# Optimization experiments

Measured on AMD Instinct MI355X. Metric: run time of the kernel, lower is better.

Reference implementation:

```python
import jax, jax.numpy as jnp
import numpy as np

B, S, D = 2, 2048, 1024
H = 16
DH = D // H
FFN = 4096
EPS = 1e-5
SCALE = 1.0 / np.sqrt(DH).astype(np.float32)


def layer_norm(x, g, b):
    mu = jnp.mean(x, axis=-1, keepdims=True)
    var = jnp.mean(jnp.square(x - mu), axis=-1, keepdims=True)
    return (x - mu) * jax.lax.rsqrt(var + EPS) * g + b


def setup_inputs() -> dict:
    key = jax.random.key(0)
    ks = jax.random.split(key, 12)
    std = 0.02
    return {
        "x": jax.random.normal(ks[0], (B, S, D), dtype=jnp.float32),
        "mask": jax.random.randint(ks[1], (B, S), 0, 2, dtype=jnp.int32),
        "w_qkv": jax.random.normal(ks[2], (D, 3 * D), dtype=jnp.float32) * std,
        "w_out": jax.random.normal(ks[3], (D, D), dtype=jnp.float32) * std,
        "b_out": jnp.zeros((D,), dtype=jnp.float32),
        "g1": jnp.ones((D,), dtype=jnp.float32),
        "be1": jnp.zeros((D,), dtype=jnp.float32),
        "g2": jnp.ones((D,), dtype=jnp.float32),
        "be2": jnp.zeros((D,), dtype=jnp.float32),
        "w1": jax.random.normal(ks[4], (D, FFN), dtype=jnp.float32) * std,
        "b1": jnp.zeros((FFN,), dtype=jnp.float32),
        "w2": jax.random.normal(ks[5], (FFN, D), dtype=jnp.float32) * std,
        "b2": jnp.zeros((D,), dtype=jnp.float32),
    }


def reference(x, mask, w_qkv, w_out, b_out, g1, be1, g2, be2, w1, b1, w2, b2):
    # --- pre-norm self-attention ---
    h = layer_norm(x, g1, be1)                              # [B,S,D]
    qkv = (h @ w_qkv).reshape(B, S, 3, H, DH)               # [B,S,3,H,Dh]
    q, k, v = [jnp.transpose(qkv[:, :, i], (0, 2, 1, 3)) for i in range(3)]  # [B,H,S,Dh]
    scores = jnp.einsum("bhqd,bhkd->bhqk", q, k) * SCALE    # [B,H,S,S]
    key_mask = (mask != 0)[:, None, None, :]                # [B,1,1,S]
    scores = jnp.where(key_mask, scores, -1e9)
    attn = jax.nn.softmax(scores, axis=-1)
    out = jnp.einsum("bhqk,bhkd->bhqd", attn, v)            # [B,H,S,Dh]
    out = jnp.transpose(out, (0, 2, 1, 3)).reshape(B, S, D)
    x = x + (out @ w_out + b_out)
    # --- pre-norm FFN ---
    h2 = layer_norm(x, g2, be2)
    ffn = jax.nn.relu(h2 @ w1 + b1) @ w2 + b2
    return x + ffn
```

## Files before the change

kernel.cpp:

```cpp
#include <hip/hip_runtime.h>

typedef unsigned short u16;
typedef __bf16 bf16x8 __attribute__((ext_vector_type(8)));
typedef float f32x4 __attribute__((ext_vector_type(4)));

typedef __attribute__((address_space(1))) const void* as1cv;
typedef __attribute__((address_space(3))) void* as3v;

__device__ __forceinline__ u16 f2bf(float f) {
  union { float f; unsigned u; } v;
  v.f = f;
  unsigned r = (v.u + 0x7fffu + ((v.u >> 16) & 1u)) >> 16;
  return (u16)r;
}

__device__ __forceinline__ unsigned cvtpk(float lo, float hi) {
  unsigned r;
  asm("v_cvt_pk_bf16_f32 %0, %1, %2" : "=v"(r) : "v"(lo), "v"(hi));
  return r;
}

__device__ __forceinline__ void gload16(const void* g, void* l) {
  __builtin_amdgcn_global_load_lds((as1cv)g, (as3v)l, 16, 0, 0);
}

__global__ __launch_bounds__(256)
void ln_kernel(const float* __restrict__ x, const float* __restrict__ g,
               const float* __restrict__ be, u16* __restrict__ out) {
  __shared__ float red[8];
  const int row = blockIdx.x;
  const int tid = threadIdx.x;
  const float4 v = ((const float4*)(x + (size_t)row * 1024))[tid];
  float s = v.x + v.y + v.z + v.w;
#pragma unroll
  for (int off = 1; off < 64; off <<= 1) s += __shfl_xor(s, off, 64);
  const int wv = tid >> 6, lane = tid & 63;
  if (lane == 0) red[wv] = s;
  __syncthreads();
  s = red[0] + red[1] + red[2] + red[3];
  const float mu = s * (1.0f / 1024.0f);
  const float d0 = v.x - mu, d1 = v.y - mu, d2 = v.z - mu, d3 = v.w - mu;
  float q = d0 * d0 + d1 * d1 + d2 * d2 + d3 * d3;
#pragma unroll
  for (int off = 1; off < 64; off <<= 1) q += __shfl_xor(q, off, 64);
  if (lane == 0) red[4 + wv] = q;
  __syncthreads();
  q = red[4] + red[5] + red[6] + red[7];
  const float inv = rsqrtf(q * (1.0f / 1024.0f) + 1e-5f);
  const float4 gv = ((const float4*)g)[tid];
  const float4 bv = ((const float4*)be)[tid];
  unsigned p0 = (unsigned)f2bf(d0 * inv * gv.x + bv.x) |
                ((unsigned)f2bf(d1 * inv * gv.y + bv.y) << 16);
  unsigned p1 = (unsigned)f2bf(d2 * inv * gv.z + bv.z) |
                ((unsigned)f2bf(d3 * inv * gv.w + bv.w) << 16);
  uint2 o; o.x = p0; o.y = p1;
  *(uint2*)(out + (size_t)row * 1024 + tid * 4) = o;
}

__global__ __launch_bounds__(256)
void transpose_all(const float* __restrict__ i0, u16* __restrict__ o0,
                   const float* __restrict__ i1, u16* __restrict__ o1,
                   const float* __restrict__ i2, u16* __restrict__ o2,
                   const float* __restrict__ i3, u16* __restrict__ o3) {
  __shared__ float t[32][33];
  int id = blockIdx.x;
  const float* in; u16* out; int K, N, nx;
  if (id < 3072)      { in = i0; out = o0; K = 1024; N = 3072; nx = 96; }
  else if (id < 4096) { id -= 3072; in = i1; out = o1; K = 1024; N = 1024; nx = 32; }
  else if (id < 8192) { id -= 4096; in = i2; out = o2; K = 1024; N = 4096; nx = 128; }
  else                { id -= 8192; in = i3; out = o3; K = 4096; N = 1024; nx = 32; }
  const int n0 = (id % nx) * 32, k0 = (id / nx) * 32;
  const int tx = threadIdx.x & 31, ty = threadIdx.x >> 5;
  for (int r = ty; r < 32; r += 8)
    t[r][tx] = in[(size_t)(k0 + r) * N + n0 + tx];
  __syncthreads();
  for (int r = ty; r < 32; r += 8)
    out[(size_t)(n0 + r) * K + k0 + tx] = f2bf(t[tx][r]);
}

__global__ __launch_bounds__(256, 3)
void gemm64(const u16* __restrict__ A, const u16* __restrict__ Bt,
            const float* __restrict__ bias, const float* __restrict__ res,
            float* __restrict__ C, int M, int N, int K) {
  __shared__ u16 As[4][4096];
  __shared__ u16 Bs[4][2048];
  const int tid = threadIdx.x;
  const int wv = tid >> 6, lane = tid & 63;
  const int bm = blockIdx.x * 128;
  const int bn = blockIdx.y * 64;
  const int wr = wv >> 1, wc = wv & 1;
  const int l16 = lane & 15, lh = lane >> 4;

  const int ssk = ((lane & 3) ^ ((lane >> 3) & 3)) << 3;
  const int rdk = (lh ^ ((l16 >> 1) & 3)) << 3;

  f32x4 acc[4][2] = {};

  const u16* Ag = A + (size_t)(bm + wv * 16 + (lane >> 2)) * K + ssk;
  const u16* Bg = Bt + (size_t)(bn + wv * 16 + (lane >> 2)) * K + ssk;

#define STG_A64(buf, ko)  do { \
    gload16(Ag + (ko), &As[buf][wv * 512]); \
    gload16(Ag + (size_t)64 * K + (ko), &As[buf][2048 + wv * 512]); } while (0)
#define STG_B64(buf, ko)  do { \
    gload16(Bg + (ko), &Bs[buf][wv * 512]); } while (0)

  const int nst = K >> 5;
  STG_A64(0, 0); STG_B64(0, 0);
  STG_A64(1, 32); STG_B64(1, 32);
  STG_A64(2, 64); STG_B64(2, 64);

  for (int t = 0; t < nst; ++t) {
    const int cur = t & 3;
    const int rem = nst - t;
    if (rem >= 3)      asm volatile("s_waitcnt vmcnt(6)" ::: "memory");
    else if (rem == 2) asm volatile("s_waitcnt vmcnt(3)" ::: "memory");
    else               asm volatile("s_waitcnt vmcnt(0)" ::: "memory");
    __builtin_amdgcn_s_barrier();
    asm volatile("" ::: "memory");
    const int nxb = (t + 3) & 3;
    bf16x8 af[4], bfv[2];
#pragma unroll
    for (int i = 0; i < 4; i++)
      af[i] = *(const bf16x8*)&As[cur][(wr * 64 + i * 16 + l16) * 32 + rdk];
    bfv[0] = *(const bf16x8*)&Bs[cur][(wc * 32 + l16) * 32 + rdk];
    if (t + 3 < nst) STG_A64(nxb, (t + 3) * 32);
    __builtin_amdgcn_s_setprio(1);
#pragma unroll
    for (int i = 0; i < 4; i++)
      acc[i][0] = __builtin_amdgcn_mfma_f32_16x16x32_bf16(af[i], bfv[0], acc[i][0], 0, 0, 0);
    __builtin_amdgcn_s_setprio(0);
    bfv[1] = *(const bf16x8*)&Bs[cur][(wc * 32 + 16 + l16) * 32 + rdk];
    if (t + 3 < nst) STG_B64(nxb, (t + 3) * 32);
    __builtin_amdgcn_s_setprio(1);
#pragma unroll
    for (int i = 0; i < 4; i++)
      acc[i][1] = __builtin_amdgcn_mfma_f32_16x16x32_bf16(af[i], bfv[1], acc[i][1], 0, 0, 0);
    __builtin_amdgcn_s_setprio(0);
  }
#undef STG_A64
#undef STG_B64

#pragma unroll
  for (int i = 0; i < 4; i++) {
#pragma unroll
    for (int j = 0; j < 2; j++) {
      const int col = bn + wc * 32 + j * 16 + l16;
      const float bv = bias[col];
#pragma unroll
      for (int r = 0; r < 4; r++) {
        const int row = bm + wr * 64 + i * 16 + lh * 4 + r;
        const float v = acc[i][j][r] + bv + res[(size_t)row * N + col];
        C[(size_t)row * N + col] = v;
      }
    }
  }
}

template<int BIAS, int RELU, int MODE>
__global__ __launch_bounds__(512, 2)
void gemm256(const u16* __restrict__ A, const u16* __restrict__ Bt,
             const float* __restrict__ bias, u16* __restrict__ C,
             u16* __restrict__ vt, int M, int N, int K) {
  __shared__ u16 As[2][16384];
  __shared__ u16 Bs[2][16384];
  const int tid = threadIdx.x;
  const int wv = tid >> 6, lane = tid & 63;
  const int l16 = lane & 15, lh = lane >> 4;
  const int wm = wv >> 2, wn = wv & 3;
  const int bm = blockIdx.x * 256, bn = blockIdx.y * 256;

  const int koff = ((lane & 7) ^ ((lane >> 3) & 7)) << 3;
  const int ka0 = ((lh ^ (l16 & 7)) << 3);
  const int ka1 = (((4 + lh) ^ (l16 & 7)) << 3);

  f32x4 acc[8][4] = {};

  const u16* Ag = A + (size_t)(bm + wv * 8 + (lane >> 3)) * K + koff;
  const u16* Bg = Bt + (size_t)(bn + wv * 8 + (lane >> 3)) * K + koff;

#define STAGE256(buf, ko)                                                  \
  do {                                                                     \
    _Pragma("unroll")                                                      \
    for (int j = 0; j < 4; ++j) {                                          \
      gload16(Ag + (size_t)(j * 64) * K + (ko), &As[buf][j * 4096 + wv * 512]); \
      gload16(Bg + (size_t)(j * 64) * K + (ko), &Bs[buf][j * 4096 + wv * 512]); \
    }                                                                      \
  } while (0)

  const int nt = K >> 6;
  STAGE256(0, 0);
  if (nt > 1) STAGE256(1, 64);

  for (int t = 0; t < nt; ++t) {
    const int cur = t & 1;
    if (t + 1 < nt) asm volatile("s_waitcnt vmcnt(8)" ::: "memory");
    else            asm volatile("s_waitcnt vmcnt(0)" ::: "memory");
    __builtin_amdgcn_s_barrier();
    asm volatile("" ::: "memory");
#pragma unroll
    for (int kk = 0; kk < 2; ++kk) {
      const int ko = kk ? ka1 : ka0;
      bf16x8 af[8], bfv[4];
#pragma unroll
      for (int i = 0; i < 8; ++i)
        af[i] = *(const bf16x8*)&As[cur][(wm * 128 + i * 16 + l16) * 64 + ko];
#pragma unroll
      for (int n = 0; n < 4; ++n)
        bfv[n] = *(const bf16x8*)&Bs[cur][(wn * 64 + n * 16 + l16) * 64 + ko];
      __builtin_amdgcn_s_setprio(1);
#pragma unroll
      for (int i = 0; i < 8; ++i)
#pragma unroll
        for (int n = 0; n < 4; ++n)
          acc[i][n] = __builtin_amdgcn_mfma_f32_16x16x32_bf16(af[i], bfv[n], acc[i][n], 0, 0, 0);
      __builtin_amdgcn_s_setprio(0);
    }
    asm volatile("" ::: "memory");
    __builtin_amdgcn_s_barrier();
    asm volatile("" ::: "memory");
    if (t + 2 < nt) STAGE256(cur, (t + 2) * 64);
  }
#undef STAGE256

#pragma unroll
  for (int i = 0; i < 8; ++i)
#pragma unroll
    for (int n = 0; n < 4; ++n) {
      const int col = bn + wn * 64 + n * 16 + l16;
      const float bv = BIAS ? bias[col] : 0.0f;
      if (MODE == 3 && bn >= 2048) {
        const int cc = col - 2048, h = cc >> 6, d = cc & 63;
        const int row0 = bm + wm * 128 + i * 16 + lh * 4;
        const int bb = row0 >> 11, kv0 = row0 & 2047;
        const int p0 = (kv0 & 32) | (((kv0 >> 2) & 3) << 3) | (((kv0 >> 4) & 1) << 2);
        uint2 o;
        o.x = (unsigned)f2bf(acc[i][n][0]) | ((unsigned)f2bf(acc[i][n][1]) << 16);
        o.y = (unsigned)f2bf(acc[i][n][2]) | ((unsigned)f2bf(acc[i][n][3]) << 16);
        *(uint2*)(vt + ((size_t)(bb * 16 + h) * 64 + d) * 2048 + (kv0 & ~63) + p0) = o;
      } else {
#pragma unroll
        for (int r = 0; r < 4; ++r) {
          const int row = bm + wm * 128 + i * 16 + lh * 4 + r;
          float v = acc[i][n][r] + bv;
          if (RELU) v = fmaxf(v, 0.0f);
          C[(size_t)row * N + col] = f2bf(v);
        }
      }
    }
}

__global__ __launch_bounds__(256, 4)
void attn3(const u16* __restrict__ qkv, const u16* __restrict__ vT,
           const int* __restrict__ mask, u16* __restrict__ aout) {
  __shared__ u16 KsS[2][4096];
  __shared__ u16 VsS[2][4096];
  __shared__ float mbL[2048];

  const int tid = threadIdx.x;
  const int wv = tid >> 6, lane = tid & 63;
  const int l16 = lane & 15, lh = lane >> 4;
  const int bh = blockIdx.x, b = bh >> 4, h = bh & 15;
  const int q0 = blockIdx.y * 64 + wv * 16;

  {
    const int4* srcm = (const int4*)(mask + b * 2048);
    float4* dstm = (float4*)mbL;
#pragma unroll
    for (int u = 0; u < 2; ++u) {
      const int4 mv = srcm[tid + u * 256];
      float4 f;
      f.x = mv.x ? 0.f : -1.4426950408889634e9f;
      f.y = mv.y ? 0.f : -1.4426950408889634e9f;
      f.z = mv.z ? 0.f : -1.4426950408889634e9f;
      f.w = mv.w ? 0.f : -1.4426950408889634e9f;
      dstm[tid + u * 256] = f;
    }
  }

  bf16x8 qf[2];
#pragma unroll
  for (int c = 0; c < 2; ++c)
    qf[c] = *(const bf16x8*)(qkv + (size_t)(b * 2048 + q0 + l16) * 3072 + h * 64 + c * 32 + 8 * lh);

  const int rs = (l16 & 7) << 4;
  const int koff0 = ((16 * lh) ^ rs) >> 1;
  const int koff1 = ((64 + 16 * lh) ^ rs) >> 1;
  const int voff0 = koff0, voff1 = koff1;

  const int rl0 = wv * 8 + (lane >> 3);
  const int rl1 = 32 + wv * 8 + (lane >> 3);
  const int glog = (lane & 7) ^ ((lane >> 3) & 7);
  const u16* kg0 = qkv + (size_t)(b * 2048 + rl0) * 3072 + 1024 + h * 64 + 8 * glog;
  const u16* kg1 = qkv + (size_t)(b * 2048 + rl1) * 3072 + 1024 + h * 64 + 8 * glog;
  const u16* vg0 = vT + ((size_t)bh * 64 + rl0) * 2048 + 8 * glog;
  const u16* vg1 = vT + ((size_t)bh * 64 + rl1) * 2048 + 8 * glog;

  gload16(kg0, &KsS[0][wv * 512]);
  gload16(kg1, &KsS[0][2048 + wv * 512]);
  gload16(vg0, &VsS[0][wv * 512]);
  gload16(vg1, &VsS[0][2048 + wv * 512]);
  kg0 += 64 * 3072; kg1 += 64 * 3072; vg0 += 64; vg1 += 64;

  const float CL2 = 0.125f * 1.4426950408889634f;
  f32x4 lsum = {};
  f32x4 oT[4] = {};
  union U8 { unsigned u[4]; bf16x8 v; };
  U8 onesu;
  onesu.u[0] = onesu.u[1] = onesu.u[2] = onesu.u[3] = 0x3F803F80u;
  const bf16x8 ones = onesu.v;

  for (int t = 0; t < 32; ++t) {
    asm volatile("s_waitcnt vmcnt(0)" ::: "memory");
    __syncthreads();
    const int cur = t & 1;
    if (t + 1 < 32) {
      const int nx = cur ^ 1;
      gload16(kg0, &KsS[nx][wv * 512]);
      gload16(kg1, &KsS[nx][2048 + wv * 512]);
      gload16(vg0, &VsS[nx][wv * 512]);
      gload16(vg1, &VsS[nx][2048 + wv * 512]);
      kg0 += 64 * 3072; kg1 += 64 * 3072; vg0 += 64; vg1 += 64;
    }

    const u16* Kb = &KsS[cur][0];
    const u16* Vb = &VsS[cur][0];

    f32x4 mbc[4];
#pragma unroll
    for (int n = 0; n < 4; ++n)
      mbc[n] = *(const f32x4*)&mbL[t * 64 + n * 16 + 4 * lh];

    f32x4 s[4] = {};
    __builtin_amdgcn_s_setprio(1);
#pragma unroll
    for (int c = 0; c < 2; ++c) {
      const int ko = c ? koff1 : koff0;
      bf16x8 kf[4];
#pragma unroll
      for (int n = 0; n < 4; ++n)
        kf[n] = *(const bf16x8*)(Kb + (n * 16 + l16) * 64 + ko);
#pragma unroll
      for (int n = 0; n < 4; ++n)
        s[n] = __builtin_amdgcn_mfma_f32_16x16x32_bf16(kf[n], qf[c], s[n], 0, 0, 0);
    }
    __builtin_amdgcn_s_setprio(0);

#pragma unroll
    for (int n = 0; n < 4; ++n)
#pragma unroll
      for (int j = 0; j < 4; ++j)
        s[n][j] = __builtin_exp2f(fmaf(s[n][j], CL2, mbc[n][j]));

    U8 pa[2];
#pragma unroll
    for (int u = 0; u < 2; ++u) {
      pa[u].u[0] = cvtpk(s[2 * u][0], s[2 * u][1]);
      pa[u].u[1] = cvtpk(s[2 * u][2], s[2 * u][3]);
      pa[u].u[2] = cvtpk(s[2 * u + 1][0], s[2 * u + 1][1]);
      pa[u].u[3] = cvtpk(s[2 * u + 1][2], s[2 * u + 1][3]);
    }

    __builtin_amdgcn_s_setprio(1);
#pragma unroll
    for (int u = 0; u < 2; ++u) {
      const int vo = u ? voff1 : voff0;
      lsum = __builtin_amdgcn_mfma_f32_16x16x32_bf16(ones, pa[u].v, lsum, 0, 0, 0);
#pragma unroll
      for (int D = 0; D < 4; ++D) {
        const bf16x8 va = *(const bf16x8*)(Vb + (D * 16 + l16) * 64 + vo);
        oT[D] = __builtin_amdgcn_mfma_f32_16x16x32_bf16(va, pa[u].v, oT[D], 0, 0, 0);
      }
    }
    __builtin_amdgcn_s_setprio(0);
  }

  const float rr = 1.0f / lsum[0];
#pragma unroll
  for (int D = 0; D < 4; ++D) {
    uint2 o;
    o.x = cvtpk(oT[D][0] * rr, oT[D][1] * rr);
    o.y = cvtpk(oT[D][2] * rr, oT[D][3] * rr);
    *(uint2*)(aout + (size_t)(b * 2048 + q0 + l16) * 1024 + h * 64 + D * 16 + 4 * lh) = o;
  }
}

extern "C" void kernel_launch(void* const* d_in, const int* in_sizes, int n_in,
                              void* d_out, int out_size, void* d_ws, size_t ws_size,
                              hipStream_t stream) {
  (void)in_sizes; (void)n_in; (void)out_size; (void)ws_size;
  const float* x     = (const float*)d_in[0];
  const int*   mask  = (const int*)d_in[1];
  const float* w_qkv = (const float*)d_in[2];
  const float* w_out = (const float*)d_in[3];
  const float* b_out = (const float*)d_in[4];
  const float* g1    = (const float*)d_in[5];
  const float* be1   = (const float*)d_in[6];
  const float* g2    = (const float*)d_in[7];
  const float* be2   = (const float*)d_in[8];
  const float* w1    = (const float*)d_in[9];
  const float* b1    = (const float*)d_in[10];
  const float* w2    = (const float*)d_in[11];
  const float* b2    = (const float*)d_in[12];
  float* out = (float*)d_out;

  char* ws = (char*)d_ws;
  u16* hA    = (u16*)(ws);
  u16* wqkvT = (u16*)(ws + 8388608);
  u16* woutT = (u16*)(ws + 14680064);
  u16* w1T   = (u16*)(ws + 16777216);
  u16* w2T   = (u16*)(ws + 25165824);
  u16* qkv   = (u16*)(ws + 33554432);
  u16* ffn1  = (u16*)(ws + 33554432);
  u16* vTb   = (u16*)(ws + 67108864);
  u16* aout  = (u16*)(ws + 75497472);

  ln_kernel<<<4096, 256, 0, stream>>>(x, g1, be1, hA);
  transpose_all<<<12288, 256, 0, stream>>>(w_qkv, wqkvT, w_out, woutT, w1, w1T, w2, w2T);
  gemm256<0, 0, 3><<<dim3(16, 12), 512, 0, stream>>>(hA, wqkvT, nullptr, qkv, vTb, 4096, 3072, 1024);
  attn3<<<dim3(32, 32), 256, 0, stream>>>(qkv, vTb, mask, aout);
  gemm64<<<dim3(32, 16), 256, 0, stream>>>(aout, woutT, b_out, x, out, 4096, 1024, 1024);
  ln_kernel<<<4096, 256, 0, stream>>>(out, g2, be2, hA);
  gemm256<1, 1, 1><<<dim3(16, 16), 512, 0, stream>>>(hA, w1T, b1, ffn1, nullptr, 4096, 4096, 1024);
  gemm64<<<dim3(32, 16), 256, 0, stream>>>(ffn1, w2T, b2, out, out, 4096, 1024, 4096);
}
```

Before: 240.5 us.

## Process two query sub-tiles per wave in attention to reuse K/V fragments

Each wave now handles 32 query rows (two 16-row sub-tiles) instead of 16, so every block covers 128 queries and the grid along queries is halved. K and V fragments read from LDS and the staged global tiles are reused across both sub-tiles, cutting LDS reads and global K/V traffic per query. In exchange register use doubles for accumulators and scores, so launch bounds drop to two blocks per SM, and there are only half as many blocks (512) to fill the device.

```diff
diff --git a/kernel.cpp b/kernel.cpp
--- a/kernel.cpp
+++ b/kernel.cpp
@@ -250,8 +250,8 @@
     }
 }
 
-__global__ __launch_bounds__(256, 4)
-void attn3(const u16* __restrict__ qkv, const u16* __restrict__ vT,
+__global__ __launch_bounds__(256, 2)
+void attn4(const u16* __restrict__ qkv, const u16* __restrict__ vT,
            const int* __restrict__ mask, u16* __restrict__ aout) {
   __shared__ u16 KsS[2][4096];
   __shared__ u16 VsS[2][4096];
@@ -261,7 +261,7 @@
   const int wv = tid >> 6, lane = tid & 63;
   const int l16 = lane & 15, lh = lane >> 4;
   const int bh = blockIdx.x, b = bh >> 4, h = bh & 15;
-  const int q0 = blockIdx.y * 64 + wv * 16;
+  const int q0 = blockIdx.y * 128 + wv * 32;
 
   {
     const int4* srcm = (const int4*)(mask + b * 2048);
@@ -278,10 +278,12 @@
     }
   }
 
-  bf16x8 qf[2];
-#pragma unroll
-  for (int c = 0; c < 2; ++c)
-    qf[c] = *(const bf16x8*)(qkv + (size_t)(b * 2048 + q0 + l16) * 3072 + h * 64 + c * 32 + 8 * lh);
+  bf16x8 qf[2][2];
+#pragma unroll
+  for (int qb = 0; qb < 2; ++qb)
+#pragma unroll
+    for (int c = 0; c < 2; ++c)
+      qf[qb][c] = *(const bf16x8*)(qkv + (size_t)(b * 2048 + q0 + qb * 16 + l16) * 3072 + h * 64 + c * 32 + 8 * lh);
 
   const int rs = (l16 & 7) << 4;
   const int koff0 = ((16 * lh) ^ rs) >> 1;
@@ -303,8 +305,8 @@
   kg0 += 64 * 3072; kg1 += 64 * 3072; vg0 += 64; vg1 += 64;
 
   const float CL2 = 0.125f * 1.4426950408889634f;
-  f32x4 lsum = {};
-  f32x4 oT[4] = {};
+  f32x4 lsum[2] = {};
+  f32x4 oT[4][2] = {};
   union U8 { unsigned u[4]; bf16x8 v; };
   U8 onesu;
   onesu.u[0] = onesu.u[1] = onesu.u[2] = onesu.u[3] = 0x3F803F80u;
@@ -331,7 +333,7 @@
     for (int n = 0; n < 4; ++n)
       mbc[n] = *(const f32x4*)&mbL[t * 64 + n * 16 + 4 * lh];
 
-    f32x4 s[4] = {};
+    f32x4 s[2][4] = {};
     __builtin_amdgcn_s_setprio(1);
 #pragma unroll
     for (int c = 0; c < 2; ++c) {
@@ -341,47 +343,58 @@
       for (int n = 0; n < 4; ++n)
         kf[n] = *(const bf16x8*)(Kb + (n * 16 + l16) * 64 + ko);
 #pragma unroll
+      for (int qb = 0; qb < 2; ++qb)
+#pragma unroll
+        for (int n = 0; n < 4; ++n)
+          s[qb][n] = __builtin_amdgcn_mfma_f32_16x16x32_bf16(kf[n], qf[qb][c], s[qb][n], 0, 0, 0);
+    }
+    __builtin_amdgcn_s_setprio(0);
+
+#pragma unroll
+    for (int qb = 0; qb < 2; ++qb)
+#pragma unroll
       for (int n = 0; n < 4; ++n)
-        s[n] = __builtin_amdgcn_mfma_f32_16x16x32_bf16(kf[n], qf[c], s[n], 0, 0, 0);
-    }
-    __builtin_amdgcn_s_setprio(0);
-
-#pragma unroll
-    for (int n = 0; n < 4; ++n)
-#pragma unroll
-      for (int j = 0; j < 4; ++j)
-        s[n][j] = __builtin_exp2f(fmaf(s[n][j], CL2, mbc[n][j]));
-
-    U8 pa[2];
-#pragma unroll
-    for (int u = 0; u < 2; ++u) {
-      pa[u].u[0] = cvtpk(s[2 * u][0], s[2 * u][1]);
-      pa[u].u[1] = cvtpk(s[2 * u][2], s[2 * u][3]);
-      pa[u].u[2] = cvtpk(s[2 * u + 1][0], s[2 * u + 1][1]);
-      pa[u].u[3] = cvtpk(s[2 * u + 1][2], s[2 * u + 1][3]);
-    }
+#pragma unroll
+        for (int j = 0; j < 4; ++j)
+          s[qb][n][j] = __builtin_exp2f(fmaf(s[qb][n][j], CL2, mbc[n][j]));
+
+    U8 pa[2][2];
+#pragma unroll
+    for (int qb = 0; qb < 2; ++qb)
+#pragma unroll
+      for (int u = 0; u < 2; ++u) {
+        pa[qb][u].u[0] = cvtpk(s[qb][2 * u][0], s[qb][2 * u][1]);
+        pa[qb][u].u[1] = cvtpk(s[qb][2 * u][2], s[qb][2 * u][3]);
+        pa[qb][u].u[2] = cvtpk(s[qb][2 * u + 1][0], s[qb][2 * u + 1][1]);
+        pa[qb][u].u[3] = cvtpk(s[qb][2 * u + 1][2], s[qb][2 * u + 1][3]);
+      }
 
     __builtin_amdgcn_s_setprio(1);
 #pragma unroll
     for (int u = 0; u < 2; ++u) {
       const int vo = u ? voff1 : voff0;
-      lsum = __builtin_amdgcn_mfma_f32_16x16x32_bf16(ones, pa[u].v, lsum, 0, 0, 0);
+      lsum[0] = __builtin_amdgcn_mfma_f32_16x16x32_bf16(ones, pa[0][u].v, lsum[0], 0, 0, 0);
+      lsum[1] = __builtin_amdgcn_mfma_f32_16x16x32_bf16(ones, pa[1][u].v, lsum[1], 0, 0, 0);
 #pragma unroll
       for (int D = 0; D < 4; ++D) {
         const bf16x8 va = *(const bf16x8*)(Vb + (D * 16 + l16) * 64 + vo);
-        oT[D] = __builtin_amdgcn_mfma_f32_16x16x32_bf16(va, pa[u].v, oT[D], 0, 0, 0);
+        oT[D][0] = __builtin_amdgcn_mfma_f32_16x16x32_bf16(va, pa[0][u].v, oT[D][0], 0, 0, 0);
+        oT[D][1] = __builtin_amdgcn_mfma_f32_16x16x32_bf16(va, pa[1][u].v, oT[D][1], 0, 0, 0);
       }
     }
     __builtin_amdgcn_s_setprio(0);
   }
 
-  const float rr = 1.0f / lsum[0];
-#pragma unroll
-  for (int D = 0; D < 4; ++D) {
-    uint2 o;
-    o.x = cvtpk(oT[D][0] * rr, oT[D][1] * rr);
-    o.y = cvtpk(oT[D][2] * rr, oT[D][3] * rr);
-    *(uint2*)(aout + (size_t)(b * 2048 + q0 + l16) * 1024 + h * 64 + D * 16 + 4 * lh) = o;
+#pragma unroll
+  for (int qb = 0; qb < 2; ++qb) {
+    const float rr = 1.0f / lsum[qb][0];
+#pragma unroll
+    for (int D = 0; D < 4; ++D) {
+      uint2 o;
+      o.x = cvtpk(oT[D][qb][0] * rr, oT[D][qb][1] * rr);
+      o.y = cvtpk(oT[D][qb][2] * rr, oT[D][qb][3] * rr);
+      *(uint2*)(aout + (size_t)(b * 2048 + q0 + qb * 16 + l16) * 1024 + h * 64 + D * 16 + 4 * lh) = o;
+    }
   }
 }
 
@@ -418,7 +431,7 @@
   ln_kernel<<<4096, 256, 0, stream>>>(x, g1, be1, hA);
   transpose_all<<<12288, 256, 0, stream>>>(w_qkv, wqkvT, w_out, woutT, w1, w1T, w2, w2T);
   gemm256<0, 0, 3><<<dim3(16, 12), 512, 0, stream>>>(hA, wqkvT, nullptr, qkv, vTb, 4096, 3072, 1024);
-  attn3<<<dim3(32, 32), 256, 0, stream>>>(qkv, vTb, mask, aout);
+  attn4<<<dim3(32, 16), 256, 0, stream>>>(qkv, vTb, mask, aout);
   gemm64<<<dim3(32, 16), 256, 0, stream>>>(aout, woutT, b_out, x, out, 4096, 1024, 1024);
   ln_kernel<<<4096, 256, 0, stream>>>(out, g2, be2, hA);
   gemm256<1, 1, 1><<<dim3(16, 16), 512, 0, stream>>>(hA, w1T, b1, ffn1, nullptr, 4096, 4096, 1024);
```

After: 239.9 us, median of 3. About the same (-0.3%).
